# Kernel optimization log

Measured on AMD Instinct MI355X. Metric: run time of the kernel, lower is better.

The kernel has to match this reference:

```python
import jax, jax.numpy as jnp
import numpy as np

NEG_SLOPE = 0.01  # torch nn.LeakyReLU default
N_NODES = 100000
N_EDGES = 500000
IN_DIM, OUT_DIM, EF_DIM, EMB_DIM = 128, 128, 64, 256


def leaky_relu(x):
    return jnp.where(x >= 0, x, NEG_SLOPE * x)


def setup_inputs() -> dict:
    key = jax.random.key(0)
    ks = jax.random.split(key, 8)
    s = 0.05
    nf = jax.random.normal(ks[0], (N_NODES, IN_DIM), dtype=jnp.float32)
    ef = jax.random.normal(ks[1], (N_EDGES, EF_DIM), dtype=jnp.float32)
    src = jax.random.randint(ks[2], (N_EDGES,), 0, N_NODES, dtype=jnp.int32)
    dst = jax.random.randint(ks[3], (N_EDGES,), 0, N_NODES, dtype=jnp.int32)
    # Linear weights stored as (in, out); y = x @ W. No biases (bias=False).
    We1 = jax.random.normal(ks[4], (2 * IN_DIM + EF_DIM, EMB_DIM), dtype=jnp.float32) * s
    We2 = jax.random.normal(ks[5], (EMB_DIM, OUT_DIM), dtype=jnp.float32) * s
    Wn1 = jax.random.normal(ks[6], (IN_DIM + OUT_DIM, EMB_DIM), dtype=jnp.float32) * s
    Wn2 = jax.random.normal(ks[7], (EMB_DIM, OUT_DIM), dtype=jnp.float32) * s
    return {"nf": nf, "ef": ef, "src": src, "dst": dst,
            "We1": We1, "We2": We2, "Wn1": Wn1, "Wn2": Wn2}


def reference(nf, ef, src, dst, We1, We2, Wn1, Wn2):
    # Symmetrize: add reversed edges carrying the same edge features.
    src_full = jnp.concatenate([src, dst])            # [2E]
    dst_full = jnp.concatenate([dst, src])            # [2E]
    ef_full = jnp.concatenate([ef, ef], axis=0)       # [2E, ef_dim]

    # message_func: MLP over [src_nf | dst_nf | ef]
    edge_in = jnp.concatenate([nf[src_full], nf[dst_full], ef_full], axis=-1)  # [2E, 2*in+ef]
    msg = leaky_relu(edge_in @ We1) @ We2              # [2E, out]

    # reduce_func: sum messages per destination node (zeros for isolated nodes)
    red = jax.ops.segment_sum(msg, dst_full, num_segments=nf.shape[0])  # [N, out]

    # apply_node_func: MLP over [nf | red_msg]
    node_in = jnp.concatenate([nf, red], axis=-1)      # [N, in+out]
    out_nf = leaky_relu(node_in @ Wn1) @ Wn2           # [N, out]
    return out_nf
```

## Files before the change

kernel.cpp:

```cpp
#include <hip/hip_runtime.h>
#include <hip/hip_bf16.h>
#include <string.h>


using f32x4  = __attribute__((ext_vector_type(4))) float;
using bf16x8 = __attribute__((ext_vector_type(8))) short;

#define LROW 72
#define CSROW 264
#define YROW 132
#define P128 132
#define P256 264

__device__ __forceinline__ float lrelu(float x) { return x >= 0.f ? x : 0.01f * x; }

__device__ __forceinline__ ushort f2bf(float f) {
    union { float f; unsigned u; } v; v.f = f;
    unsigned u = v.u;
    return (ushort)((u + 0x7fffu + ((u >> 16) & 1u)) >> 16);
}
__device__ __forceinline__ float bf2f(ushort u) {
    union { unsigned u; float f; } v; v.u = ((unsigned)u) << 16; return v.f;
}

__device__ __forceinline__ void atomic_pk_add_bf16(void* addr, unsigned val) {
    asm volatile("global_atomic_pk_add_bf16 %0, %1, off" : : "v"(addr), "v"(val) : "memory");
}

__global__ __launch_bounds__(256) void gemm_ab(
    const ushort* __restrict__ X,
    const ushort* __restrict__ Wt,
    ushort* __restrict__ out)
{
    __shared__ ushort Xs[128 * P128];
    const int tid  = threadIdx.x;
    const int lane = tid & 63;
    const int wv   = tid >> 6;
    const int wm   = wv >> 1, wn = wv & 1;
    const int row0 = blockIdx.x * 128;

    #pragma unroll
    for (int q = 0; q < 8; ++q) {
        int idx = q * 256 + tid;
        int r = idx >> 4, c = idx & 15;
        *reinterpret_cast<uint4*>(&Xs[r * P128 + c * 8]) =
            *reinterpret_cast<const uint4*>(X + (size_t)(row0 + r) * 128 + c * 8);
    }
    __syncthreads();

    const int g8 = (lane >> 4) * 8;
    for (int cb = 0; cb < 4; ++cb) {
        f32x4 acc[4][4] = {};
        #pragma unroll
        for (int ks = 0; ks < 4; ++ks) {
            bf16x8 af[4], bf[4];
            #pragma unroll
            for (int i = 0; i < 4; ++i) {
                int mrow = wm * 64 + i * 16 + (lane & 15);
                af[i] = *reinterpret_cast<const bf16x8*>(&Xs[mrow * P128 + ks * 32 + g8]);
                int nc = cb * 128 + wn * 64 + i * 16 + (lane & 15);
                bf[i] = *reinterpret_cast<const bf16x8*>(Wt + (size_t)nc * 128 + ks * 32 + g8);
            }
            #pragma unroll
            for (int i = 0; i < 4; ++i)
                #pragma unroll
                for (int j = 0; j < 4; ++j)
                    acc[i][j] = __builtin_amdgcn_mfma_f32_16x16x32_bf16(af[i], bf[j], acc[i][j], 0, 0, 0);
        }
        #pragma unroll
        for (int i = 0; i < 4; ++i) {
            int gr0 = row0 + wm * 64 + i * 16 + ((lane >> 4) << 2);
            #pragma unroll
            for (int j = 0; j < 4; ++j) {
                int gc = cb * 128 + wn * 64 + j * 16 + (lane & 15);
                #pragma unroll
                for (int r = 0; r < 4; ++r)
                    out[(size_t)(gr0 + r) * 512 + gc] = f2bf(acc[i][j][r]);
            }
        }
    }
}

__global__ __launch_bounds__(256) void edge_proj(
    const ushort* __restrict__ efb,
    const ushort* __restrict__ Wet,
    const ushort* __restrict__ We2t,
    const ushort* __restrict__ AB,
    const int* __restrict__ src, const int* __restrict__ dst,
    ushort* __restrict__ H,
    int E)
{
    __shared__ ushort Cs[128 * YROW];
    __shared__ ushort efs[64 * LROW];
    __shared__ int sd[128];

    const int tid  = threadIdx.x;
    const int lane = tid & 63;
    const int wv   = tid >> 6;
    const int wm   = wv >> 1, wn = wv & 1;
    const int eb   = blockIdx.x * 64;
    const int g8   = (lane >> 4) * 8;

    #pragma unroll
    for (int q = 0; q < 2; ++q) {
        int idx = q * 256 + tid;
        int r = idx >> 3, c = (idx & 7) * 8;
        *reinterpret_cast<uint4*>(&efs[r * LROW + c]) =
            *reinterpret_cast<const uint4*>(efb + (size_t)(eb + r) * 64 + c);
    }
    if (tid < 64)       sd[tid] = (eb + tid < E) ? src[eb + tid] : -1;
    else if (tid < 128) sd[tid] = (eb + tid - 64 < E) ? dst[eb + tid - 64] : -1;
    __syncthreads();

    f32x4 accc[4][4] = {};
    #pragma unroll
    for (int ks = 0; ks < 2; ++ks) {
        bf16x8 af[4], bf[4];
        #pragma unroll
        for (int i = 0; i < 4; ++i) {
            int er = i * 16 + (lane & 15);
            af[i] = *reinterpret_cast<const bf16x8*>(&efs[er * LROW + ks * 32 + g8]);
            int nc = wv * 64 + i * 16 + (lane & 15);
            bf[i] = *reinterpret_cast<const bf16x8*>(Wet + (size_t)nc * 64 + ks * 32 + g8);
        }
        #pragma unroll
        for (int i = 0; i < 4; ++i)
            #pragma unroll
            for (int j = 0; j < 4; ++j)
                accc[i][j] = __builtin_amdgcn_mfma_f32_16x16x32_bf16(af[i], bf[j], accc[i][j], 0, 0, 0);
    }
    #pragma unroll
    for (int i = 0; i < 4; ++i) {
        int er0 = i * 16 + ((lane >> 4) << 2);
        #pragma unroll
        for (int j = 0; j < 4; ++j) {
            int fc = wv * 64 + j * 16 + (lane & 15);
            #pragma unroll
            for (int r = 0; r < 4; ++r)
                Cs[(er0 + r) * CSROW + fc] = f2bf(accc[i][j][r]);
        }
    }
    __syncthreads();

    f32x4 acc[4][4] = {};
    #pragma unroll
    for (int ks = 0; ks < 8; ++ks) {
        bf16x8 mf[4], wf[4];
        #pragma unroll
        for (int i = 0; i < 4; ++i) {
            int el = i * 16 + (lane & 15);
            int a_ = wm ? sd[64 + el] : sd[el];
            int b_ = wm ? sd[el]      : sd[64 + el];
            if (a_ < 0) a_ = 0;
            if (b_ < 0) b_ = 0;
            int k = ks * 32 + g8;
            bf16x8 a8 = *reinterpret_cast<const bf16x8*>(AB + (size_t)a_ * 512 + k);
            bf16x8 b8 = *reinterpret_cast<const bf16x8*>(AB + (size_t)b_ * 512 + 256 + k);
            bf16x8 c8 = *reinterpret_cast<const bf16x8*>(&Cs[el * CSROW + k]);
            bf16x8 m8;
            #pragma unroll
            for (int t = 0; t < 8; ++t) {
                float f = lrelu(bf2f((ushort)a8[t]) + bf2f((ushort)b8[t]) + bf2f((ushort)c8[t]));
                m8[t] = (short)f2bf(f);
            }
            mf[i] = m8;
        }
        #pragma unroll
        for (int j = 0; j < 4; ++j) {
            int nc = wn * 64 + j * 16 + (lane & 15);
            wf[j] = *reinterpret_cast<const bf16x8*>(We2t + (size_t)nc * 256 + ks * 32 + g8);
        }
        #pragma unroll
        for (int i = 0; i < 4; ++i)
            #pragma unroll
            for (int j = 0; j < 4; ++j)
                acc[i][j] = __builtin_amdgcn_mfma_f32_16x16x32_bf16(mf[i], wf[j], acc[i][j], 0, 0, 0);
    }
    __syncthreads();

    ushort* Ys = Cs;
    #pragma unroll
    for (int i = 0; i < 4; ++i) {
        int yr0 = wm * 64 + i * 16 + ((lane >> 4) << 2);
        #pragma unroll
        for (int j = 0; j < 4; ++j) {
            int yc = wn * 64 + j * 16 + (lane & 15);
            #pragma unroll
            for (int r = 0; r < 4; ++r)
                Ys[(yr0 + r) * YROW + yc] = f2bf(acc[i][j][r]);
        }
    }
    __syncthreads();

    #pragma unroll
    for (int q = 0; q < 32; ++q) {
        int row = wv * 32 + q;
        int node = (row < 64) ? sd[64 + row] : sd[row - 64];
        if (node < 0) continue;
        ushort2 yv = *(const ushort2*)(&Ys[row * YROW + lane * 2]);
        unsigned uv; memcpy(&uv, &yv, 4);
        atomic_pk_add_bf16(H + (size_t)node * 128 + lane * 2, uv);
    }
}

__global__ __launch_bounds__(256) void mlp_fused(
    const ushort* __restrict__ H,
    const ushort* __restrict__ nfb,
    const ushort* __restrict__ Wn1t,
    const ushort* __restrict__ Wn2t,
    float* __restrict__ out, int Nreal)
{
    __shared__ ushort lds[128 * P256];
    ushort* Ns  = lds;
    ushort* Rs  = lds + 128 * P128;
    ushort* Hid = lds;

    const int tid  = threadIdx.x;
    const int lane = tid & 63;
    const int wv   = tid >> 6;
    const int wm   = wv >> 1, wn = wv & 1;
    const int row0 = blockIdx.x * 128;
    const int g8   = (lane >> 4) * 8;

    #pragma unroll
    for (int q = 0; q < 8; ++q) {
        int idx = q * 256 + tid;
        int r = idx >> 4, c = (idx & 15) * 8;
        *reinterpret_cast<uint4*>(&Ns[r * P128 + c]) =
            *reinterpret_cast<const uint4*>(nfb + (size_t)(row0 + r) * 128 + c);
        *reinterpret_cast<uint4*>(&Rs[r * P128 + c]) =
            *reinterpret_cast<const uint4*>(H + (size_t)(row0 + r) * 128 + c);
    }
    __syncthreads();

    f32x4 a2[2][4][4] = {};
    #pragma unroll
    for (int cb = 0; cb < 2; ++cb) {
        #pragma unroll
        for (int ks = 0; ks < 8; ++ks) {
            bf16x8 af[4], bf[4];
            #pragma unroll
            for (int i = 0; i < 4; ++i) {
                int mrow = wm * 64 + i * 16 + (lane & 15);
                af[i] = (ks < 4)
                    ? *reinterpret_cast<const bf16x8*>(&Ns[mrow * P128 + ks * 32 + g8])
                    : *reinterpret_cast<const bf16x8*>(&Rs[mrow * P128 + (ks - 4) * 32 + g8]);
                int nc = cb * 128 + wn * 64 + i * 16 + (lane & 15);
                bf[i] = *reinterpret_cast<const bf16x8*>(Wn1t + (size_t)nc * 256 + ks * 32 + g8);
            }
            #pragma unroll
            for (int i = 0; i < 4; ++i)
                #pragma unroll
                for (int j = 0; j < 4; ++j)
                    a2[cb][i][j] = __builtin_amdgcn_mfma_f32_16x16x32_bf16(af[i], bf[j], a2[cb][i][j], 0, 0, 0);
        }
    }
    __syncthreads();

    #pragma unroll
    for (int cb = 0; cb < 2; ++cb)
        #pragma unroll
        for (int i = 0; i < 4; ++i) {
            int er0 = wm * 64 + i * 16 + ((lane >> 4) << 2);
            #pragma unroll
            for (int j = 0; j < 4; ++j) {
                int fc = cb * 128 + wn * 64 + j * 16 + (lane & 15);
                #pragma unroll
                for (int r = 0; r < 4; ++r)
                    Hid[(er0 + r) * P256 + fc] = f2bf(lrelu(a2[cb][i][j][r]));
            }
        }
    __syncthreads();

    f32x4 a3[4][4] = {};
    #pragma unroll
    for (int ks = 0; ks < 8; ++ks) {
        bf16x8 af[4], bf[4];
        #pragma unroll
        for (int i = 0; i < 4; ++i) {
            int mrow = wm * 64 + i * 16 + (lane & 15);
            af[i] = *reinterpret_cast<const bf16x8*>(&Hid[mrow * P256 + ks * 32 + g8]);
            int nc = wn * 64 + i * 16 + (lane & 15);
            bf[i] = *reinterpret_cast<const bf16x8*>(Wn2t + (size_t)nc * 256 + ks * 32 + g8);
        }
        #pragma unroll
        for (int i = 0; i < 4; ++i)
            #pragma unroll
            for (int j = 0; j < 4; ++j)
                a3[i][j] = __builtin_amdgcn_mfma_f32_16x16x32_bf16(af[i], bf[j], a3[i][j], 0, 0, 0);
    }
    #pragma unroll
    for (int i = 0; i < 4; ++i) {
        int gr0 = row0 + wm * 64 + i * 16 + ((lane >> 4) << 2);
        #pragma unroll
        for (int j = 0; j < 4; ++j) {
            int gc = wn * 64 + j * 16 + (lane & 15);
            #pragma unroll
            for (int r = 0; r < 4; ++r) {
                int gr = gr0 + r;
                if (gr < Nreal) out[(size_t)gr * 128 + gc] = a3[i][j][r];
            }
        }
    }
}

__global__ __launch_bounds__(256) void cvt_pad(
    const float* __restrict__ x, ushort* __restrict__ y, size_t n_real, size_t n_pad)
{
    size_t i = ((size_t)blockIdx.x * 256 + threadIdx.x) * 4;
    if (i >= n_pad) return;
    ushort4 o;
    if (i < n_real) {
        float4 v = *(const float4*)(x + i);
        o.x = f2bf(v.x); o.y = f2bf(v.y); o.z = f2bf(v.z); o.w = f2bf(v.w);
    } else { o.x = 0; o.y = 0; o.z = 0; o.w = 0; }
    *(ushort4*)(y + i) = o;
}

__global__ __launch_bounds__(256) void wcvt(
    const float* __restrict__ We1, const float* __restrict__ We2,
    const float* __restrict__ Wn1, const float* __restrict__ Wn2,
    ushort* __restrict__ Wabt, ushort* __restrict__ Wet, ushort* __restrict__ We2t,
    ushort* __restrict__ Wn1t, ushort* __restrict__ Wn2t)
{
    int idx = blockIdx.x * 256 + threadIdx.x;
    switch (blockIdx.y) {
    case 0: if (idx < 256*128) { int n = idx >> 7, k = idx & 127; Wabt[idx]            = f2bf(We1[k * 256 + n]); } break;
    case 1: if (idx < 256*128) { int n = idx >> 7, k = idx & 127; Wabt[32768 + idx]    = f2bf(We1[(128 + k) * 256 + n]); } break;
    case 2: if (idx < 256*64)  { int n = idx >> 6, k = idx & 63;  Wet[idx]             = f2bf(We1[(256 + k) * 256 + n]); } break;
    case 3: if (idx < 128*256) { int n = idx >> 8, k = idx & 255; We2t[idx]            = f2bf(We2[k * 128 + n]); } break;
    case 4: if (idx < 256*256) { int n = idx >> 8, k = idx & 255; Wn1t[idx]            = f2bf(Wn1[k * 256 + n]); } break;
    case 5: if (idx < 128*256) { int n = idx >> 8, k = idx & 255; Wn2t[idx]            = f2bf(Wn2[k * 128 + n]); } break;
    }
}

extern "C" void kernel_launch(void* const* d_in, const int* in_sizes, int n_in,
                              void* d_out, int out_size, void* d_ws, size_t ws_size,
                              hipStream_t stream) {
    const float* nf  = (const float*)d_in[0];
    const float* ef  = (const float*)d_in[1];
    const int*   src = (const int*)d_in[2];
    const int*   dst = (const int*)d_in[3];
    const float* We1 = (const float*)d_in[4];
    const float* We2 = (const float*)d_in[5];
    const float* Wn1 = (const float*)d_in[6];
    const float* Wn2 = (const float*)d_in[7];
    float* out = (float*)d_out;

    const int  N  = in_sizes[0] / 128;
    const int  E  = in_sizes[2];
    const int  Np = (N + 127) & ~127;
    const long Ep = ((long)E + 127) & ~127L;

    char* p = (char*)d_ws;
    auto alloc = [&](size_t bytes) { char* r = p; p += (bytes + 255) & ~(size_t)255; return r; };
    ushort* AB   = (ushort*)alloc((size_t)Np * 512 * 2);
    ushort* H    = (ushort*)alloc((size_t)Np * 128 * 2);
    ushort* nfb  = (ushort*)alloc((size_t)Np * 128 * 2);
    ushort* efb  = (ushort*)alloc((size_t)Ep * 64 * 2);
    ushort* Wabt = (ushort*)alloc(65536 * 2);
    ushort* Wet  = (ushort*)alloc(16384 * 2);
    ushort* We2t = (ushort*)alloc(32768 * 2);
    ushort* Wn1t = (ushort*)alloc(65536 * 2);
    ushort* Wn2t = (ushort*)alloc(32768 * 2);

    dim3 blk(256);

    wcvt<<<dim3(256, 6), blk, 0, stream>>>(We1, We2, Wn1, Wn2, Wabt, Wet, We2t, Wn1t, Wn2t);
    cvt_pad<<<dim3((unsigned)((size_t)Np * 128 / 1024)), blk, 0, stream>>>(nf, nfb, (size_t)N * 128, (size_t)Np * 128);
    cvt_pad<<<dim3((unsigned)((size_t)Ep * 64 / 1024)), blk, 0, stream>>>(ef, efb, (size_t)E * 64, (size_t)Ep * 64);

    gemm_ab<<<dim3(Np / 128), blk, 0, stream>>>(nfb, Wabt, AB);

    hipMemsetAsync(H, 0, (size_t)Np * 128 * 2, stream);

    edge_proj<<<dim3((unsigned)(Ep / 64)), blk, 0, stream>>>(
        efb, Wet, We2t, AB, src, dst, H, E);

    mlp_fused<<<dim3(Np / 128), blk, 0, stream>>>(H, nfb, Wn1t, Wn2t, out, N);
}
```

Baseline: 914.0 us.

## Restructure edge kernel: 32 edges per block, coalesced message build in LDS

The edge kernel now handles 32 edges (64 directed messages) per block instead of 64. It first builds the full leaky-ReLU message matrix in shared memory with row-contiguous, wave-per-message gathers of the AB rows, then runs the second GEMM from LDS. Before, each MFMA lane gathered scattered 16-byte pieces of AB rows inside the K loop. The edge-feature projection is computed once per edge and reused for both directions, and blocks double in number with smaller tiles. The aim is better-coalesced gathers and higher occupancy, at the cost of a separate LDS staging pass and one more barrier.

```diff
diff --git a/kernel.cpp b/kernel.cpp
--- a/kernel.cpp
+++ b/kernel.cpp
@@ -6,11 +6,9 @@
 using f32x4  = __attribute__((ext_vector_type(4))) float;
 using bf16x8 = __attribute__((ext_vector_type(8))) short;
 
-#define LROW 72
-#define CSROW 264
-#define YROW 132
 #define P128 132
 #define P256 264
+#define YROW 132
 
 __device__ __forceinline__ float lrelu(float x) { return x >= 0.f ? x : 0.01f * x; }
 
@@ -81,7 +79,7 @@
     }
 }
 
-__global__ __launch_bounds__(256) void edge_proj(
+__global__ __launch_bounds__(256) void edge_msg(
     const ushort* __restrict__ efb,
     const ushort* __restrict__ Wet,
     const ushort* __restrict__ We2t,
@@ -90,112 +88,119 @@
     ushort* __restrict__ H,
     int E)
 {
-    __shared__ ushort Cs[128 * YROW];
-    __shared__ ushort efs[64 * LROW];
-    __shared__ int sd[128];
+    __shared__ ushort Ms[64 * P256];
+    __shared__ ushort Cs[32 * P256];
+    __shared__ int own_s[64], oth_s[64];
 
     const int tid  = threadIdx.x;
     const int lane = tid & 63;
     const int wv   = tid >> 6;
-    const int wm   = wv >> 1, wn = wv & 1;
-    const int eb   = blockIdx.x * 64;
+    const int eb   = blockIdx.x * 32;
     const int g8   = (lane >> 4) * 8;
 
-    #pragma unroll
-    for (int q = 0; q < 2; ++q) {
-        int idx = q * 256 + tid;
-        int r = idx >> 3, c = (idx & 7) * 8;
-        *reinterpret_cast<uint4*>(&efs[r * LROW + c]) =
-            *reinterpret_cast<const uint4*>(efb + (size_t)(eb + r) * 64 + c);
-    }
-    if (tid < 64)       sd[tid] = (eb + tid < E) ? src[eb + tid] : -1;
-    else if (tid < 128) sd[tid] = (eb + tid - 64 < E) ? dst[eb + tid - 64] : -1;
-    __syncthreads();
-
-    f32x4 accc[4][4] = {};
+    if (tid < 32) {
+        int e = eb + tid;
+        int s_ = (e < E) ? src[e] : -1;
+        int d_ = (e < E) ? dst[e] : -1;
+        own_s[tid]      = d_;
+        oth_s[tid]      = (s_ < 0) ? 0 : s_;
+        own_s[32 + tid] = s_;
+        oth_s[32 + tid] = (d_ < 0) ? 0 : d_;
+    }
+
+    f32x4 ac[2][4] = {};
     #pragma unroll
     for (int ks = 0; ks < 2; ++ks) {
-        bf16x8 af[4], bf[4];
-        #pragma unroll
-        for (int i = 0; i < 4; ++i) {
+        bf16x8 af[2], bf[4];
+        #pragma unroll
+        for (int i = 0; i < 2; ++i) {
             int er = i * 16 + (lane & 15);
-            af[i] = *reinterpret_cast<const bf16x8*>(&efs[er * LROW + ks * 32 + g8]);
-            int nc = wv * 64 + i * 16 + (lane & 15);
-            bf[i] = *reinterpret_cast<const bf16x8*>(Wet + (size_t)nc * 64 + ks * 32 + g8);
-        }
-        #pragma unroll
-        for (int i = 0; i < 4; ++i)
+            af[i] = *reinterpret_cast<const bf16x8*>(efb + (size_t)(eb + er) * 64 + ks * 32 + g8);
+        }
+        #pragma unroll
+        for (int j = 0; j < 4; ++j) {
+            int nc = wv * 64 + j * 16 + (lane & 15);
+            bf[j] = *reinterpret_cast<const bf16x8*>(Wet + (size_t)nc * 64 + ks * 32 + g8);
+        }
+        #pragma unroll
+        for (int i = 0; i < 2; ++i)
             #pragma unroll
             for (int j = 0; j < 4; ++j)
-                accc[i][j] = __builtin_amdgcn_mfma_f32_16x16x32_bf16(af[i], bf[j], accc[i][j], 0, 0, 0);
-    }
-    #pragma unroll
-    for (int i = 0; i < 4; ++i) {
+                ac[i][j] = __builtin_amdgcn_mfma_f32_16x16x32_bf16(af[i], bf[j], ac[i][j], 0, 0, 0);
+    }
+    #pragma unroll
+    for (int i = 0; i < 2; ++i) {
         int er0 = i * 16 + ((lane >> 4) << 2);
         #pragma unroll
         for (int j = 0; j < 4; ++j) {
             int fc = wv * 64 + j * 16 + (lane & 15);
             #pragma unroll
             for (int r = 0; r < 4; ++r)
-                Cs[(er0 + r) * CSROW + fc] = f2bf(accc[i][j][r]);
-        }
-    }
-    __syncthreads();
-
-    f32x4 acc[4][4] = {};
+                Cs[(er0 + r) * P256 + fc] = f2bf(ac[i][j][r]);
+        }
+    }
+    __syncthreads();
+
+    #pragma unroll 4
+    for (int p = 0; p < 16; ++p) {
+        int m   = p * 4 + wv;
+        int oth = oth_s[m];
+        int own = own_s[m];
+        int ownc = (own < 0) ? 0 : own;
+        int rc  = m & 31;
+        #pragma unroll
+        for (int h = 0; h < 2; ++h) {
+            int c = h * 128 + lane * 2;
+            ushort2 av = *(const ushort2*)(AB + (size_t)oth  * 512 + c);
+            ushort2 bv = *(const ushort2*)(AB + (size_t)ownc * 512 + 256 + c);
+            ushort2 cv = *(const ushort2*)(&Cs[rc * P256 + c]);
+            ushort2 mv;
+            mv.x = f2bf(lrelu(bf2f(av.x) + bf2f(bv.x) + bf2f(cv.x)));
+            mv.y = f2bf(lrelu(bf2f(av.y) + bf2f(bv.y) + bf2f(cv.y)));
+            *(ushort2*)(&Ms[m * P256 + c]) = mv;
+        }
+    }
+    __syncthreads();
+
+    const int wm = wv >> 1, wn = wv & 1;
+    f32x4 ay[2][4] = {};
     #pragma unroll
     for (int ks = 0; ks < 8; ++ks) {
-        bf16x8 mf[4], wf[4];
-        #pragma unroll
-        for (int i = 0; i < 4; ++i) {
-            int el = i * 16 + (lane & 15);
-            int a_ = wm ? sd[64 + el] : sd[el];
-            int b_ = wm ? sd[el]      : sd[64 + el];
-            if (a_ < 0) a_ = 0;
-            if (b_ < 0) b_ = 0;
-            int k = ks * 32 + g8;
-            bf16x8 a8 = *reinterpret_cast<const bf16x8*>(AB + (size_t)a_ * 512 + k);
-            bf16x8 b8 = *reinterpret_cast<const bf16x8*>(AB + (size_t)b_ * 512 + 256 + k);
-            bf16x8 c8 = *reinterpret_cast<const bf16x8*>(&Cs[el * CSROW + k]);
-            bf16x8 m8;
-            #pragma unroll
-            for (int t = 0; t < 8; ++t) {
-                float f = lrelu(bf2f((ushort)a8[t]) + bf2f((ushort)b8[t]) + bf2f((ushort)c8[t]));
-                m8[t] = (short)f2bf(f);
-            }
-            mf[i] = m8;
+        bf16x8 af[2], bf[4];
+        #pragma unroll
+        for (int i = 0; i < 2; ++i) {
+            int mrow = wm * 32 + i * 16 + (lane & 15);
+            af[i] = *reinterpret_cast<const bf16x8*>(&Ms[mrow * P256 + ks * 32 + g8]);
         }
         #pragma unroll
         for (int j = 0; j < 4; ++j) {
             int nc = wn * 64 + j * 16 + (lane & 15);
-            wf[j] = *reinterpret_cast<const bf16x8*>(We2t + (size_t)nc * 256 + ks * 32 + g8);
-        }
-        #pragma unroll
-        for (int i = 0; i < 4; ++i)
+            bf[j] = *reinterpret_cast<const bf16x8*>(We2t + (size_t)nc * 256 + ks * 32 + g8);
+        }
+        #pragma unroll
+        for (int i = 0; i < 2; ++i)
             #pragma unroll
             for (int j = 0; j < 4; ++j)
-                acc[i][j] = __builtin_amdgcn_mfma_f32_16x16x32_bf16(mf[i], wf[j], acc[i][j], 0, 0, 0);
-    }
-    __syncthreads();
-
+                ay[i][j] = __builtin_amdgcn_mfma_f32_16x16x32_bf16(af[i], bf[j], ay[i][j], 0, 0, 0);
+    }
     ushort* Ys = Cs;
     #pragma unroll
-    for (int i = 0; i < 4; ++i) {
-        int yr0 = wm * 64 + i * 16 + ((lane >> 4) << 2);
+    for (int i = 0; i < 2; ++i) {
+        int yr0 = wm * 32 + i * 16 + ((lane >> 4) << 2);
         #pragma unroll
         for (int j = 0; j < 4; ++j) {
             int yc = wn * 64 + j * 16 + (lane & 15);
             #pragma unroll
             for (int r = 0; r < 4; ++r)
-                Ys[(yr0 + r) * YROW + yc] = f2bf(acc[i][j][r]);
-        }
-    }
-    __syncthreads();
-
-    #pragma unroll
-    for (int q = 0; q < 32; ++q) {
-        int row = wv * 32 + q;
-        int node = (row < 64) ? sd[64 + row] : sd[row - 64];
+                Ys[(yr0 + r) * YROW + yc] = f2bf(ay[i][j][r]);
+        }
+    }
+    __syncthreads();
+
+    #pragma unroll 4
+    for (int q = 0; q < 16; ++q) {
+        int row  = wv * 16 + q;
+        int node = own_s[row];
         if (node < 0) continue;
         ushort2 yv = *(const ushort2*)(&Ys[row * YROW + lane * 2]);
         unsigned uv; memcpy(&uv, &yv, 4);
@@ -374,7 +379,7 @@
 
     hipMemsetAsync(H, 0, (size_t)Np * 128 * 2, stream);
 
-    edge_proj<<<dim3((unsigned)(Ep / 64)), blk, 0, stream>>>(
+    edge_msg<<<dim3((unsigned)(Ep / 32)), blk, 0, stream>>>(
         efb, Wet, We2t, AB, src, dst, H, E);
 
     mlp_fused<<<dim3(Np / 128), blk, 0, stream>>>(H, nfb, Wn1t, Wn2t, out, N);
```

Measured after the change: 771.5 us. 1.18x faster.
